# Performance work log

Hardware: AMD Instinct MI355X
Metric: run time of the kernel (lower is better)

The kernel has to match this reference:

```python
import jax, jax.numpy as jnp
import numpy as np

B, M, HS, K = 2, 2048, 1024, 16
D = HS // K


def setup_inputs() -> dict:
    key = jax.random.key(0)
    k1, k2, k3, k4 = jax.random.split(key, 4)
    s = 1.0 / np.sqrt(HS)
    return {
        "h": jax.random.normal(k1, (B, M, HS), jnp.float32),
        "W_span": jax.random.normal(k2, (2 * K, HS), jnp.float32) * s,
        "W_val": jax.random.normal(k3, (HS, HS), jnp.float32) * s,
        "W_out": jax.random.normal(k4, (HS, HS), jnp.float32) * s,
    }


def _head_reshape(x, d):
    # (B, M, K*d) -> (B*K, M, d), matching torch view/transpose in head_reshape
    b, m, _ = x.shape
    return x.reshape(b, m, K, d).transpose(0, 2, 1, 3).reshape(b * K, m, d)


def reference(h, W_span, W_val, W_out):
    b, m, hs = h.shape
    span = _head_reshape(h @ W_span.T, 2)        # (B*K, M, 2)
    value = _head_reshape(h @ W_val.T, D)        # (B*K, M, D)
    # AutoSelectAttention: learned per-position Gaussian span over absolute positions
    pos = jnp.arange(m, dtype=h.dtype)           # (M,)
    mean = jax.nn.sigmoid(span[..., 0]) * m      # (B*K, M) span center in [0, M]
    soft = jax.nn.softplus(span[..., 1])         # (B*K, M) sharpness >= 0
    diff = pos[None, None, :] - mean[..., None]  # (B*K, M, M)
    scores = -soft[..., None] * (diff * diff)
    attn = jax.nn.softmax(scores, axis=-1)       # (B*K, M, M)
    out = jnp.matmul(attn, value)                # (B*K, M, D)
    out = out.reshape(b, K, m, D).transpose(0, 2, 1, 3).reshape(b, m, hs)
    return out @ W_out.T
```

## Files before the change

### kernel.cpp

```cpp
#include <hip/hip_runtime.h>
#include <hip/hip_bf16.h>

#define MM   2048
#define HSZ  1024
#define KH   16
#define DH   64

typedef __attribute__((ext_vector_type(8))) short bf16x8;
typedef __attribute__((ext_vector_type(4))) float f32x4;
typedef __attribute__((ext_vector_type(8))) unsigned short u16x8;

#define GLOAD_LDS16(gp, lp) \
    __builtin_amdgcn_global_load_lds( \
        (const __attribute__((address_space(1))) unsigned int*)(gp), \
        (__attribute__((address_space(3))) unsigned int*)(lp), 16, 0, 0)

__device__ __forceinline__ unsigned short f2bf(float x) {
    union { float f; unsigned u; } v; v.f = x;
    unsigned r = v.u + 0x7FFFu + ((v.u >> 16) & 1u);
    return (unsigned short)(r >> 16);
}

__global__ __launch_bounds__(256) void span_cvt(
    const float* __restrict__ h, const float* __restrict__ Wspan,
    const float* __restrict__ Wval, const float* __restrict__ Wout,
    float* __restrict__ mean_, float* __restrict__ soft_,
    unsigned short* __restrict__ h_bf,
    unsigned short* __restrict__ Wval_bf, unsigned short* __restrict__ Wout_bf)
{
    __shared__ float hrow[4][HSZ];
    int t = threadIdx.x;

    if (blockIdx.x >= 1024) {
        int bid = blockIdx.x - 1024;
        const float* in = (bid < 1024) ? Wval : Wout;
        unsigned short* out = (bid < 1024) ? Wval_bf : Wout_bf;
        int i = ((bid & 1023) * 256 + t) * 4;
        float4 v = *(const float4*)(in + i);
        ushort4 o;
        o.x = f2bf(v.x); o.y = f2bf(v.y); o.z = f2bf(v.z); o.w = f2bf(v.w);
        *(ushort4*)(out + i) = o;
        return;
    }

    int row0 = blockIdx.x * 4;
    #pragma unroll
    for (int i = 0; i < 4; ++i) {
        int li = t + 256 * i;
        int r = li >> 8, c4 = (li & 255) * 4;
        float4 hv = *(const float4*)&h[(long)(row0 + r) * HSZ + c4];
        *(float4*)&hrow[r][c4] = hv;
        ushort4 hb;
        hb.x = f2bf(hv.x); hb.y = f2bf(hv.y); hb.z = f2bf(hv.z); hb.w = f2bf(hv.w);
        *(ushort4*)&h_bf[(long)(row0 + r) * HSZ + c4] = hb;
    }
    __syncthreads();
    int o = t >> 3, part = t & 7;
    const float* w = Wspan + o * HSZ;
    float4 acc[4] = {};
    #pragma unroll 4
    for (int i = 0; i < 32; ++i) {
        int c = part * 4 + i * 32;
        float4 wv = *(const float4*)&w[c];
        #pragma unroll
        for (int r = 0; r < 4; ++r) {
            float4 a = *(const float4*)&hrow[r][c];
            acc[r].x += a.x * wv.x; acc[r].y += a.y * wv.y;
            acc[r].z += a.z * wv.z; acc[r].w += a.w * wv.w;
        }
    }
    #pragma unroll
    for (int r = 0; r < 4; ++r) {
        float s = acc[r].x + acc[r].y + acc[r].z + acc[r].w;
        s += __shfl_xor(s, 1, 64);
        s += __shfl_xor(s, 2, 64);
        s += __shfl_xor(s, 4, 64);
        if (part == 0) {
            int m = row0 + r;
            int b = m >> 11, mm = m & 2047;
            int bk = b * KH + (o >> 1);
            if ((o & 1) == 0) {
                mean_[bk * MM + mm] = (1.f / (1.f + __expf(-s))) * (float)MM;
            } else {
                float sp = (s > 15.f) ? s : log1pf(__expf(s));
                soft_[bk * MM + mm] = sp;
            }
        }
    }
}

#define SROW(li) ((li) >> 3)
#define SCOL(li) ((((li) & 7) ^ (SROW(li) & 7)) * 8)

template<int STORE_BF16>
__device__ __forceinline__ void gemm_core64(
    unsigned short* __restrict__ AsB, unsigned short* __restrict__ BsB,
    const unsigned short* __restrict__ A, const unsigned short* __restrict__ Bm,
    void* __restrict__ Cv, int N, int Kd,
    int bx, int by, int bz, long aZ, long bZ, long cZ)
{
    const unsigned short* Ab = A  + bz * aZ;
    const unsigned short* Bb = Bm + bz * bZ;
    long czoff = bz * cZ;
    int row0 = by * 64;
    int col0 = bx * 64;
    int t = threadIdx.x;
    int wid = t >> 6, l = t & 63;
    int wr = wid >> 1, wc = wid & 1;
    int lr = l & 15, lhi = l >> 4;

    #define STAGE64(buf, k0s) do { \
        unsigned short* As_ = AsB + (buf) * 4096; \
        unsigned short* Bs_ = BsB + (buf) * 4096; \
        int a0 = t, a1 = t + 256; \
        GLOAD_LDS16(Ab + (long)(row0 + SROW(a0)) * Kd + (k0s) + SCOL(a0), As_ + a0 * 8); \
        GLOAD_LDS16(Ab + (long)(row0 + SROW(a1)) * Kd + (k0s) + SCOL(a1), As_ + a1 * 8); \
        GLOAD_LDS16(Bb + (long)(col0 + SROW(a0)) * Kd + (k0s) + SCOL(a0), Bs_ + a0 * 8); \
        GLOAD_LDS16(Bb + (long)(col0 + SROW(a1)) * Kd + (k0s) + SCOL(a1), Bs_ + a1 * 8); \
    } while (0)

    f32x4 acc[2][2] = {};
    int nk = Kd >> 6;

    STAGE64(0, 0);

    for (int ks = 0; ks < nk; ++ks) {
        int cur = ks & 1;
        if (ks + 1 < nk) {
            STAGE64(cur ^ 1, (ks + 1) << 6);
            asm volatile("s_waitcnt vmcnt(4)" ::: "memory");
        } else {
            asm volatile("s_waitcnt vmcnt(0)" ::: "memory");
        }
        __builtin_amdgcn_s_barrier();

        bf16x8 af[2][2], bfr[2][2];
        #pragma unroll
        for (int kk = 0; kk < 2; ++kk) {
            int slotx = ((kk * 4 + lhi) ^ (lr & 7)) << 3;
            #pragma unroll
            for (int i = 0; i < 2; ++i)
                af[kk][i] = *(const bf16x8*)(AsB + cur * 4096 + (wr * 32 + i * 16 + lr) * 64 + slotx);
            #pragma unroll
            for (int j = 0; j < 2; ++j)
                bfr[kk][j] = *(const bf16x8*)(BsB + cur * 4096 + (wc * 32 + j * 16 + lr) * 64 + slotx);
        }
        asm volatile("s_waitcnt lgkmcnt(0)" ::: "memory");
        __builtin_amdgcn_sched_barrier(0);
        __builtin_amdgcn_s_barrier();

        #pragma unroll
        for (int kk = 0; kk < 2; ++kk)
            #pragma unroll
            for (int i = 0; i < 2; ++i)
                #pragma unroll
                for (int j = 0; j < 2; ++j)
                    acc[i][j] = __builtin_amdgcn_mfma_f32_16x16x32_bf16(af[kk][i], bfr[kk][j], acc[i][j], 0, 0, 0);
    }
    #undef STAGE64

    #pragma unroll
    for (int i = 0; i < 2; ++i) {
        int rbase = row0 + wr * 32 + i * 16 + lhi * 4;
        #pragma unroll
        for (int j = 0; j < 2; ++j) {
            int cidx = col0 + wc * 32 + j * 16 + lr;
            #pragma unroll
            for (int r_ = 0; r_ < 4; ++r_) {
                long idx = czoff + (long)(rbase + r_) * N + cidx;
                if (STORE_BF16) ((unsigned short*)Cv)[idx] = f2bf(acc[i][j][r_]);
                else            ((float*)Cv)[idx] = acc[i][j][r_];
            }
        }
    }
}

__device__ void sort_core(char* smem, const float* __restrict__ mean_,
                          int* __restrict__ perm, int bk)
{
    unsigned short (*hist)[257] = (unsigned short(*)[257])smem;
    int* binTot = (int*)(smem + 16448);
    int* binStart = binTot + 32;
    int t = threadIdx.x;
    int bins[8];
    #pragma unroll
    for (int i = 0; i < 8; ++i) {
        float mq = mean_[bk * MM + t * 8 + i];
        int b = (int)(mq * (1.f / 64.f));
        bins[i] = min(31, max(0, b));
    }
    for (int b = 0; b < 32; ++b) hist[b][t] = 0;
    __syncthreads();
    #pragma unroll
    for (int i = 0; i < 8; ++i) hist[bins[i]][t]++;
    __syncthreads();
    int w = t >> 6, l = t & 63;
    for (int b = w * 8; b < w * 8 + 8; ++b) {
        int carry = 0;
        for (int g = 0; g < 4; ++g) {
            int v = (int)hist[b][g * 64 + l];
            int x = v;
            #pragma unroll
            for (int off = 1; off < 64; off <<= 1) {
                int y = __shfl_up(x, off, 64);
                if (l >= off) x += y;
            }
            hist[b][g * 64 + l] = (unsigned short)(x - v + carry);
            carry += __shfl(x, 63, 64);
        }
        if (l == 0) binTot[b] = carry;
    }
    __syncthreads();
    if (t == 0) {
        int s = 0;
        for (int b = 0; b < 32; ++b) { binStart[b] = s; s += binTot[b]; }
    }
    __syncthreads();
    #pragma unroll
    for (int i = 0; i < 8; ++i) {
        int b = bins[i];
        int prior = 0;
        #pragma unroll
        for (int j = 0; j < 8; ++j) if (j < i && bins[j] == b) prior++;
        int pos = binStart[b] + (int)hist[b][t] + prior;
        perm[bk * MM + pos] = t * 8 + i;
    }
}

__global__ __launch_bounds__(256) void vgemm_sort(
    const unsigned short* __restrict__ Wval_bf, const unsigned short* __restrict__ h_bf,
    unsigned short* __restrict__ hvT,
    const float* __restrict__ mean_, int* __restrict__ perm)
{
    __shared__ __align__(16) char smem[32768];
    int f = blockIdx.x;
    if (f < 1024) {
        int swz = (f & 7) * 128 + (f >> 3);
        int by = swz & 15, r = swz >> 4;
        int bx = r & 31, bz = r >> 5;
        gemm_core64<1>((unsigned short*)smem, (unsigned short*)(smem + 16384),
                       Wval_bf, h_bf, hvT, MM, HSZ, bx, by, bz,
                       0L, (long)MM * HSZ, (long)HSZ * MM);
    } else {
        sort_core(smem, mean_, perm, f - 1024);
    }
}

__global__ __launch_bounds__(256) void ogemm(
    const unsigned short* __restrict__ att, const unsigned short* __restrict__ Wout_bf,
    float* __restrict__ out)
{
    __shared__ __align__(16) unsigned short As[2][4096];
    __shared__ __align__(16) unsigned short Bs[2][4096];
    int f = blockIdx.x;
    int swz = (f & 7) * 128 + (f >> 3);
    int bx = swz & 15, by = (swz >> 4) & 63;
    gemm_core64<0>(&As[0][0], &Bs[0][0], att, Wout_bf, out, HSZ, HSZ,
                   bx, by, 0, 0L, 0L, 0L);
}

__global__ __launch_bounds__(512) void attn_gauss(
    const float* __restrict__ mean_, const float* __restrict__ soft_,
    const int* __restrict__ perm,
    const unsigned short* __restrict__ hvT, unsigned short* __restrict__ att)
{
    __shared__ __align__(16) unsigned short Vs[2][64 * 64];
    __shared__ float red[2][8];
    int flat = blockIdx.x;
    int swz = (flat & 7) * 64 + (flat >> 3);
    int bk = swz >> 4;
    int qb = swz & 15;
    int t = threadIdx.x, wid = t >> 6, l = t & 63;
    int b = bk >> 4, head = bk & 15;
    int lr = l & 15, lhi = l >> 4;
    int slot = qb * 128 + wid * 16 + lr;
    int q = perm[bk * MM + slot];
    float mq  = mean_[bk * MM + q];
    float sq  = soft_[bk * MM + q];
    const unsigned short* Vbase = hvT + (long)bk * DH * MM;

    float w = __fsqrt_rn(50.f / sq);
    float lo = mq - w, hi = mq + w;
    #pragma unroll
    for (int off = 1; off < 64; off <<= 1) {
        lo = fminf(lo, __shfl_xor(lo, off, 64));
        hi = fmaxf(hi, __shfl_xor(hi, off, 64));
    }
    if (l == 0) { red[0][wid] = lo; red[1][wid] = hi; }
    __syncthreads();
    float blo = red[0][0], bhi = red[1][0];
    #pragma unroll
    for (int i = 1; i < 8; ++i) {
        blo = fminf(blo, red[0][i]);
        bhi = fmaxf(bhi, red[1][i]);
    }
    blo = fmaxf(blo, 0.f);
    bhi = fmaxf(fminf(bhi, 2047.f), 0.f);
    int kt0 = ((int)blo) >> 6;
    int kt1 = ((int)bhi) >> 6;
    if (kt1 < kt0) kt1 = kt0;

    int sr = t >> 3;
    int sc = (((t & 7) ^ (sr & 7)) * 8);

    f32x4 acc[4] = {};
    float lsum = 0.f;
    int jlane0 = lhi * 8;

    GLOAD_LDS16(Vbase + (long)sr * MM + (kt0 << 6) + sc, &Vs[0][t * 8]);
    __syncthreads();

    for (int kt = kt0; kt <= kt1; ++kt) {
        int cur = (kt - kt0) & 1;
        int k0 = kt << 6;
        if (kt < kt1)
            GLOAD_LDS16(Vbase + (long)sr * MM + (k0 + 64) + sc, &Vs[cur ^ 1][t * 8]);

        float dmin = fmaxf(fmaxf((float)k0 - mq, mq - (float)(k0 + 63)), 0.f);
        bool active = (sq * dmin * dmin) < 50.f;
        if (__ballot(active)) {
            #pragma unroll
            for (int kk = 0; kk < 64; kk += 32) {
                bf16x8 pfrag;
                float dbase = (float)(k0 + kk + jlane0) - mq;
                #pragma unroll
                for (int jj = 0; jj < 8; ++jj) {
                    float d_ = dbase + (float)jj;
                    float p = __expf(-sq * d_ * d_);
                    lsum += p;
                    pfrag[jj] = (short)f2bf(p);
                }
                int slotx = (((kk >> 3) + lhi) ^ (lr & 7)) << 3;
                #pragma unroll
                for (int df = 0; df < 4; ++df) {
                    bf16x8 vf = *(const bf16x8*)&Vs[cur][(df * 16 + lr) * 64 + slotx];
                    acc[df] = __builtin_amdgcn_mfma_f32_16x16x32_bf16(pfrag, vf, acc[df], 0, 0, 0);
                }
            }
        }
        __syncthreads();
    }

    lsum += __shfl_xor(lsum, 16, 64);
    lsum += __shfl_xor(lsum, 32, 64);

    int slot_base = qb * 128 + wid * 16;
    #pragma unroll
    for (int r_ = 0; r_ < 4; ++r_) {
        int qr = lhi * 4 + r_;
        float inv = 1.f / __shfl(lsum, qr, 64);
        int qo = perm[bk * MM + slot_base + qr];
        long orow = ((long)b * MM + qo) * HSZ + head * DH;
        #pragma unroll
        for (int df = 0; df < 4; ++df)
            att[orow + df * 16 + lr] = f2bf(acc[df][r_] * inv);
    }
}

extern "C" void kernel_launch(void* const* d_in, const int* in_sizes, int n_in,
                              void* d_out, int out_size, void* d_ws, size_t ws_size,
                              hipStream_t stream) {
    (void)in_sizes; (void)n_in; (void)out_size; (void)ws_size;
    const float* h     = (const float*)d_in[0];
    const float* Wspan = (const float*)d_in[1];
    const float* Wval  = (const float*)d_in[2];
    const float* Wout  = (const float*)d_in[3];
    float* out = (float*)d_out;

    char* ws = (char*)d_ws;
    unsigned short* h_bf    = (unsigned short*)(ws);
    unsigned short* Wval_bf = (unsigned short*)(ws +  8388608);
    unsigned short* Wout_bf = (unsigned short*)(ws + 10485760);
    unsigned short* hvT     = (unsigned short*)(ws + 12582912);
    unsigned short* att     = (unsigned short*)(ws + 20971520);
    float*          mean_   = (float*)(ws + 29360128);
    float*          soft_   = (float*)(ws + 29622272);
    int*            perm    = (int*)(ws + 29884416);

    span_cvt<<<3072, 256, 0, stream>>>(h, Wspan, Wval, Wout,
                                       mean_, soft_, h_bf, Wval_bf, Wout_bf);

    vgemm_sort<<<1056, 256, 0, stream>>>(Wval_bf, h_bf, hvT, mean_, perm);

    attn_gauss<<<512, 512, 0, stream>>>(mean_, soft_, perm, hvT, att);

    ogemm<<<1024, 256, 0, stream>>>(att, Wout_bf, out);
}
```

Baseline: 66.39 us.

## Compute span projection with split-bf16 MFMA and shrink conversion grid

Replaces the scalar FP32 dot-product span projection with MFMA 16x16x32 bf16 instructions. It keeps near-FP32 accuracy by splitting h and W_span into hi and lo bf16 parts and issuing three MFMAs per step, with W_span staged in swizzled LDS. The launch drops from 3072 to 256 blocks: 128 blocks handle 32 rows each, and 128 blocks convert the weights with a 16-iteration loop. This cuts instruction count and launch overhead, at the cost of 128 KB of LDS per block, which limits occupancy.

Result: slower. 68.96 us (+3.9%).

```diff
diff --git a/kernel.cpp b/kernel.cpp
--- a/kernel.cpp
+++ b/kernel.cpp
@@ -28,63 +28,108 @@
     unsigned short* __restrict__ h_bf,
     unsigned short* __restrict__ Wval_bf, unsigned short* __restrict__ Wout_bf)
 {
-    __shared__ float hrow[4][HSZ];
+    __shared__ __align__(16) unsigned short Whi[32768];
+    __shared__ __align__(16) unsigned short Wlo[32768];
     int t = threadIdx.x;
 
-    if (blockIdx.x >= 1024) {
-        int bid = blockIdx.x - 1024;
-        const float* in = (bid < 1024) ? Wval : Wout;
-        unsigned short* out = (bid < 1024) ? Wval_bf : Wout_bf;
-        int i = ((bid & 1023) * 256 + t) * 4;
-        float4 v = *(const float4*)(in + i);
-        ushort4 o;
-        o.x = f2bf(v.x); o.y = f2bf(v.y); o.z = f2bf(v.z); o.w = f2bf(v.w);
-        *(ushort4*)(out + i) = o;
+    if (blockIdx.x >= 128) {
+        int bid = blockIdx.x - 128;
+        #pragma unroll 4
+        for (int it = 0; it < 16; ++it) {
+            int fi = bid * 256 + t + it * 32768;
+            const float* in; unsigned short* out; int off;
+            if (fi < 262144) { in = Wval; out = Wval_bf; off = fi; }
+            else             { in = Wout; out = Wout_bf; off = fi - 262144; }
+            float4 v = *(const float4*)(in + (long)off * 4);
+            ushort4 o4;
+            o4.x = f2bf(v.x); o4.y = f2bf(v.y); o4.z = f2bf(v.z); o4.w = f2bf(v.w);
+            *(ushort4*)(out + (long)off * 4) = o4;
+        }
         return;
     }
 
-    int row0 = blockIdx.x * 4;
-    #pragma unroll
-    for (int i = 0; i < 4; ++i) {
-        int li = t + 256 * i;
-        int r = li >> 8, c4 = (li & 255) * 4;
-        float4 hv = *(const float4*)&h[(long)(row0 + r) * HSZ + c4];
-        *(float4*)&hrow[r][c4] = hv;
-        ushort4 hb;
-        hb.x = f2bf(hv.x); hb.y = f2bf(hv.y); hb.z = f2bf(hv.z); hb.w = f2bf(hv.w);
-        *(ushort4*)&h_bf[(long)(row0 + r) * HSZ + c4] = hb;
-    }
-    __syncthreads();
-    int o = t >> 3, part = t & 7;
-    const float* w = Wspan + o * HSZ;
-    float4 acc[4] = {};
-    #pragma unroll 4
-    for (int i = 0; i < 32; ++i) {
-        int c = part * 4 + i * 32;
-        float4 wv = *(const float4*)&w[c];
-        #pragma unroll
-        for (int r = 0; r < 4; ++r) {
-            float4 a = *(const float4*)&hrow[r][c];
-            acc[r].x += a.x * wv.x; acc[r].y += a.y * wv.y;
-            acc[r].z += a.z * wv.z; acc[r].w += a.w * wv.w;
-        }
-    }
-    #pragma unroll
-    for (int r = 0; r < 4; ++r) {
-        float s = acc[r].x + acc[r].y + acc[r].z + acc[r].w;
-        s += __shfl_xor(s, 1, 64);
-        s += __shfl_xor(s, 2, 64);
-        s += __shfl_xor(s, 4, 64);
-        if (part == 0) {
-            int m = row0 + r;
-            int b = m >> 11, mm = m & 2047;
-            int bk = b * KH + (o >> 1);
-            if ((o & 1) == 0) {
-                mean_[bk * MM + mm] = (1.f / (1.f + __expf(-s))) * (float)MM;
-            } else {
-                float sp = (s > 15.f) ? s : log1pf(__expf(s));
-                soft_[bk * MM + mm] = sp;
-            }
+    #pragma unroll
+    for (int g = 0; g < 16; ++g) {
+        int idx = t + 256 * g;
+        int o = idx >> 7, kc = idx & 127;
+        const float* wp = Wspan + o * 1024 + kc * 8;
+        float4 w0 = *(const float4*)wp;
+        float4 w1 = *(const float4*)(wp + 4);
+        float wf[8] = {w0.x, w0.y, w0.z, w0.w, w1.x, w1.y, w1.z, w1.w};
+        u16x8 hv_, lv_;
+        #pragma unroll
+        for (int jj = 0; jj < 8; ++jj) {
+            unsigned short hu = f2bf(wf[jj]);
+            union { unsigned u; float f; } c; c.u = (unsigned)hu << 16;
+            hv_[jj] = hu;
+            lv_[jj] = f2bf(wf[jj] - c.f);
+        }
+        int slot = (o * 128 + (kc ^ (o & 7))) * 8;
+        *(u16x8*)&Whi[slot] = hv_;
+        *(u16x8*)&Wlo[slot] = lv_;
+    }
+    __syncthreads();
+
+    int wid = t >> 6, l = t & 63;
+    int lr = l & 15, lhi = l >> 4;
+    int rgrp = wid >> 1, jt = wid & 1;
+    int arow = blockIdx.x * 32 + rgrp * 16 + lr;
+    const float* hp = h + (long)arow * HSZ;
+    unsigned short* hbp = h_bf + (long)arow * HSZ;
+    int o = jt * 16 + lr;
+    int wbase = o * 128, osw = o & 7;
+
+    f32x4 acc = {};
+
+    #define PROC(a, b, ks_) do { \
+        float af_[8] = {(a).x, (a).y, (a).z, (a).w, (b).x, (b).y, (b).z, (b).w}; \
+        bf16x8 hh_, hl_; \
+        _Pragma("unroll") \
+        for (int jj = 0; jj < 8; ++jj) { \
+            unsigned short hu_ = f2bf(af_[jj]); \
+            union { unsigned u; float f; } c_; c_.u = (unsigned)hu_ << 16; \
+            hh_[jj] = (short)hu_; \
+            hl_[jj] = (short)f2bf(af_[jj] - c_.f); \
+        } \
+        if (jt == 0) *(bf16x8*)(hbp + (ks_) * 32 + lhi * 8) = hh_; \
+        int kc_ = (ks_) * 4 + lhi; \
+        int slot_ = (wbase + (kc_ ^ osw)) * 8; \
+        bf16x8 whi_ = *(const bf16x8*)&Whi[slot_]; \
+        bf16x8 wlo_ = *(const bf16x8*)&Wlo[slot_]; \
+        acc = __builtin_amdgcn_mfma_f32_16x16x32_bf16(hh_, whi_, acc, 0, 0, 0); \
+        acc = __builtin_amdgcn_mfma_f32_16x16x32_bf16(hh_, wlo_, acc, 0, 0, 0); \
+        acc = __builtin_amdgcn_mfma_f32_16x16x32_bf16(hl_, whi_, acc, 0, 0, 0); \
+    } while (0)
+
+    float4 A0a = *(const float4*)(hp + lhi * 8);
+    float4 A0b = *(const float4*)(hp + lhi * 8 + 4);
+    float4 A1a = *(const float4*)(hp + 32 + lhi * 8);
+    float4 A1b = *(const float4*)(hp + 32 + lhi * 8 + 4);
+    for (int ks = 0; ks < 32; ks += 2) {
+        float4 N0a, N0b, N1a, N1b;
+        if (ks + 2 < 32) {
+            const float* p0 = hp + (ks + 2) * 32 + lhi * 8;
+            const float* p1 = hp + (ks + 3) * 32 + lhi * 8;
+            N0a = *(const float4*)p0; N0b = *(const float4*)(p0 + 4);
+            N1a = *(const float4*)p1; N1b = *(const float4*)(p1 + 4);
+        }
+        PROC(A0a, A0b, ks);
+        PROC(A1a, A1b, ks + 1);
+        A0a = N0a; A0b = N0b; A1a = N1a; A1b = N1b;
+    }
+    #undef PROC
+
+    #pragma unroll
+    for (int r_ = 0; r_ < 4; ++r_) {
+        int m = blockIdx.x * 32 + rgrp * 16 + lhi * 4 + r_;
+        int b = m >> 11, mm = m & 2047;
+        int bk = b * KH + (o >> 1);
+        float s = acc[r_];
+        if (!(o & 1)) {
+            mean_[bk * MM + mm] = (1.f / (1.f + __expf(-s))) * (float)MM;
+        } else {
+            float sp = (s > 15.f) ? s : log1pf(__expf(s));
+            soft_[bk * MM + mm] = sp;
         }
     }
 }
@@ -377,8 +422,8 @@
     float*          soft_   = (float*)(ws + 29622272);
     int*            perm    = (int*)(ws + 29884416);
 
-    span_cvt<<<3072, 256, 0, stream>>>(h, Wspan, Wval, Wout,
-                                       mean_, soft_, h_bf, Wval_bf, Wout_bf);
+    span_cvt<<<256, 256, 0, stream>>>(h, Wspan, Wval, Wout,
+                                      mean_, soft_, h_bf, Wval_bf, Wout_bf);
 
     vgemm_sort<<<1056, 256, 0, stream>>>(Wval_bf, h_bf, hvT, mean_, perm);
 
```

## Fuse bf16 conversion into value GEMM and move span sort into attention

Applied to the files above, without the earlier changes.

The value GEMM now loads fp32 h and W_val directly, converts them to bf16 in registers and writes them into swizzled LDS. This removes the separate h_bf/Wval_bf conversion pass and its global round trip, and the span projection runs in the same launch interleaved with the GEMM blocks. The per-head sort of span centers moves into the attention kernel, which keeps the permutation in LDS and drops one kernel launch and the perm buffer. The cost is that each of the 512 attention blocks redoes its own sort, and the GEMM loses async global-to-LDS loads in favour of register staging with full vmcnt waits. The conversion also switches to a cheaper round-half-up instead of round-to-nearest-even.

Result: slower. 100.2 us (+50.9%).

```diff
diff --git a/kernel.cpp b/kernel.cpp
--- a/kernel.cpp
+++ b/kernel.cpp
@@ -20,71 +20,167 @@
     unsigned r = v.u + 0x7FFFu + ((v.u >> 16) & 1u);
     return (unsigned short)(r >> 16);
 }
-
-__global__ __launch_bounds__(256) void span_cvt(
+__device__ __forceinline__ unsigned short f2bfu(float x) {
+    union { float f; unsigned u; } v; v.f = x;
+    return (unsigned short)((v.u + 0x8000u) >> 16);
+}
+__device__ __forceinline__ u16x8 pack8(float4 a, float4 b) {
+    u16x8 o;
+    o[0] = f2bfu(a.x); o[1] = f2bfu(a.y); o[2] = f2bfu(a.z); o[3] = f2bfu(a.w);
+    o[4] = f2bfu(b.x); o[5] = f2bfu(b.y); o[6] = f2bfu(b.z); o[7] = f2bfu(b.w);
+    return o;
+}
+
+__global__ __launch_bounds__(256) void fused1(
     const float* __restrict__ h, const float* __restrict__ Wspan,
     const float* __restrict__ Wval, const float* __restrict__ Wout,
     float* __restrict__ mean_, float* __restrict__ soft_,
-    unsigned short* __restrict__ h_bf,
-    unsigned short* __restrict__ Wval_bf, unsigned short* __restrict__ Wout_bf)
+    unsigned short* __restrict__ hvT, unsigned short* __restrict__ Wout_bf)
 {
-    __shared__ float hrow[4][HSZ];
+    __shared__ __align__(16) char smem[32768];
+    int f = blockIdx.x;
     int t = threadIdx.x;
 
-    if (blockIdx.x >= 1024) {
-        int bid = blockIdx.x - 1024;
-        const float* in = (bid < 1024) ? Wval : Wout;
-        unsigned short* out = (bid < 1024) ? Wval_bf : Wout_bf;
-        int i = ((bid & 1023) * 256 + t) * 4;
-        float4 v = *(const float4*)(in + i);
-        ushort4 o;
-        o.x = f2bf(v.x); o.y = f2bf(v.y); o.z = f2bf(v.z); o.w = f2bf(v.w);
-        *(ushort4*)(out + i) = o;
+    if (f >= 2048) {
+        int bid = f - 2048;
+        #pragma unroll
+        for (int it = 0; it < 8; ++it) {
+            int fi = bid * 2048 + t + it * 256;
+            float4 v = *(const float4*)(Wout + (long)fi * 4);
+            ushort4 o4;
+            o4.x = f2bf(v.x); o4.y = f2bf(v.y); o4.z = f2bf(v.z); o4.w = f2bf(v.w);
+            *(ushort4*)(Wout_bf + (long)fi * 4) = o4;
+        }
         return;
     }
 
-    int row0 = blockIdx.x * 4;
+    if (f & 1) {
+        float (*hrow)[HSZ] = (float(*)[HSZ])smem;
+        int row0 = (f >> 1) * 4;
+        #pragma unroll
+        for (int i = 0; i < 4; ++i) {
+            int li = t + 256 * i;
+            int r = li >> 8, c4 = (li & 255) * 4;
+            *(float4*)&hrow[r][c4] = *(const float4*)&h[(long)(row0 + r) * HSZ + c4];
+        }
+        __syncthreads();
+        int o = t >> 3, part = t & 7;
+        const float* w = Wspan + o * HSZ;
+        float4 acc[4] = {};
+        #pragma unroll 4
+        for (int i = 0; i < 32; ++i) {
+            int c = part * 4 + i * 32;
+            float4 wv = *(const float4*)&w[c];
+            #pragma unroll
+            for (int r = 0; r < 4; ++r) {
+                float4 a = *(const float4*)&hrow[r][c];
+                acc[r].x += a.x * wv.x; acc[r].y += a.y * wv.y;
+                acc[r].z += a.z * wv.z; acc[r].w += a.w * wv.w;
+            }
+        }
+        #pragma unroll
+        for (int r = 0; r < 4; ++r) {
+            float s = acc[r].x + acc[r].y + acc[r].z + acc[r].w;
+            s += __shfl_xor(s, 1, 64);
+            s += __shfl_xor(s, 2, 64);
+            s += __shfl_xor(s, 4, 64);
+            if (part == 0) {
+                int m = row0 + r;
+                int b = m >> 11, mm = m & 2047;
+                int bk = b * KH + (o >> 1);
+                if ((o & 1) == 0) {
+                    mean_[bk * MM + mm] = (1.f / (1.f + __expf(-s))) * (float)MM;
+                } else {
+                    float sp = (s > 15.f) ? s : log1pf(__expf(s));
+                    soft_[bk * MM + mm] = sp;
+                }
+            }
+        }
+        return;
+    }
+
+    unsigned short* As = (unsigned short*)smem;
+    unsigned short* Bs = (unsigned short*)(smem + 16384);
+    int g = f >> 1;
+    int swz = (g & 7) * 128 + (g >> 3);
+    int by = swz & 15; int r_ = swz >> 4;
+    int bx = r_ & 31, bz = r_ >> 5;
+    int wid = t >> 6, l = t & 63;
+    int wr = wid >> 1, wc = wid & 1;
+    int lr = l & 15, lhi = l >> 4;
+
+    int srow = t >> 2, sk = (t & 3) * 16;
+    const float* Ap = Wval + (long)(by * 64 + srow) * HSZ + sk;
+    const float* Bp = h + (long)bz * MM * HSZ + (long)(bx * 64 + srow) * HSZ + sk;
+    int c0 = (t & 3) * 2;
+    int p0 = ((c0 ^ (srow & 7)) * 8), p1 = (((c0 + 1) ^ (srow & 7)) * 8);
+    int wbase = srow * 64;
+
+    #define LOADG(RA, RB, kt) do { \
+        _Pragma("unroll") for (int j_ = 0; j_ < 4; ++j_) { \
+            RA[j_] = *(const float4*)(Ap + (kt) * 64 + j_ * 4); \
+            RB[j_] = *(const float4*)(Bp + (kt) * 64 + j_ * 4); } } while (0)
+    #define CVTW(RA, RB, buf) do { \
+        *(u16x8*)&As[(buf) * 4096 + wbase + p0] = pack8(RA[0], RA[1]); \
+        *(u16x8*)&As[(buf) * 4096 + wbase + p1] = pack8(RA[2], RA[3]); \
+        *(u16x8*)&Bs[(buf) * 4096 + wbase + p0] = pack8(RB[0], RB[1]); \
+        *(u16x8*)&Bs[(buf) * 4096 + wbase + p1] = pack8(RB[2], RB[3]); } while (0)
+
+    f32x4 acc[2][2] = {};
+    #define STEP(buf) do { \
+        bf16x8 af[2][2], bfr[2][2]; \
+        _Pragma("unroll") for (int kk = 0; kk < 2; ++kk) { \
+            int slotx = ((kk * 4 + lhi) ^ (lr & 7)) << 3; \
+            _Pragma("unroll") for (int i_ = 0; i_ < 2; ++i_) \
+                af[kk][i_] = *(const bf16x8*)&As[(buf) * 4096 + (wr * 32 + i_ * 16 + lr) * 64 + slotx]; \
+            _Pragma("unroll") for (int j_ = 0; j_ < 2; ++j_) \
+                bfr[kk][j_] = *(const bf16x8*)&Bs[(buf) * 4096 + (wc * 32 + j_ * 16 + lr) * 64 + slotx]; } \
+        asm volatile("s_waitcnt lgkmcnt(0)" ::: "memory"); \
+        __builtin_amdgcn_sched_barrier(0); \
+        _Pragma("unroll") for (int kk = 0; kk < 2; ++kk) \
+            _Pragma("unroll") for (int i_ = 0; i_ < 2; ++i_) \
+                _Pragma("unroll") for (int j_ = 0; j_ < 2; ++j_) \
+                    acc[i_][j_] = __builtin_amdgcn_mfma_f32_16x16x32_bf16(af[kk][i_], bfr[kk][j_], acc[i_][j_], 0, 0, 0); \
+    } while (0)
+
+    float4 A0[4], B0[4], A1[4], B1[4];
+    LOADG(A0, B0, 0);
+    asm volatile("s_waitcnt vmcnt(0)" ::: "memory");
+    CVTW(A0, B0, 0);
+    LOADG(A1, B1, 1);
+    __syncthreads();
+
+    for (int ks = 0; ks < 16; ks += 2) {
+        if (ks + 1 < 16) {
+            asm volatile("s_waitcnt vmcnt(0)" ::: "memory");
+            CVTW(A1, B1, 1);
+            if (ks + 2 < 16) LOADG(A0, B0, ks + 2);
+        }
+        STEP(0);
+        __syncthreads();
+        if (ks + 2 < 16) {
+            asm volatile("s_waitcnt vmcnt(0)" ::: "memory");
+            CVTW(A0, B0, 0);
+            if (ks + 3 < 16) LOADG(A1, B1, ks + 3);
+        }
+        STEP(1);
+        __syncthreads();
+    }
+    #undef LOADG
+    #undef CVTW
+    #undef STEP
+
+    long czoff = (long)bz * HSZ * MM;
+    int row0 = by * 64, col0 = bx * 64;
     #pragma unroll
-    for (int i = 0; i < 4; ++i) {
-        int li = t + 256 * i;
-        int r = li >> 8, c4 = (li & 255) * 4;
-        float4 hv = *(const float4*)&h[(long)(row0 + r) * HSZ + c4];
-        *(float4*)&hrow[r][c4] = hv;
-        ushort4 hb;
-        hb.x = f2bf(hv.x); hb.y = f2bf(hv.y); hb.z = f2bf(hv.z); hb.w = f2bf(hv.w);
-        *(ushort4*)&h_bf[(long)(row0 + r) * HSZ + c4] = hb;
-    }
-    __syncthreads();
-    int o = t >> 3, part = t & 7;
-    const float* w = Wspan + o * HSZ;
-    float4 acc[4] = {};
-    #pragma unroll 4
-    for (int i = 0; i < 32; ++i) {
-        int c = part * 4 + i * 32;
-        float4 wv = *(const float4*)&w[c];
-        #pragma unroll
-        for (int r = 0; r < 4; ++r) {
-            float4 a = *(const float4*)&hrow[r][c];
-            acc[r].x += a.x * wv.x; acc[r].y += a.y * wv.y;
-            acc[r].z += a.z * wv.z; acc[r].w += a.w * wv.w;
-        }
-    }
-    #pragma unroll
-    for (int r = 0; r < 4; ++r) {
-        float s = acc[r].x + acc[r].y + acc[r].z + acc[r].w;
-        s += __shfl_xor(s, 1, 64);
-        s += __shfl_xor(s, 2, 64);
-        s += __shfl_xor(s, 4, 64);
-        if (part == 0) {
-            int m = row0 + r;
-            int b = m >> 11, mm = m & 2047;
-            int bk = b * KH + (o >> 1);
-            if ((o & 1) == 0) {
-                mean_[bk * MM + mm] = (1.f / (1.f + __expf(-s))) * (float)MM;
-            } else {
-                float sp = (s > 15.f) ? s : log1pf(__expf(s));
-                soft_[bk * MM + mm] = sp;
-            }
+    for (int i = 0; i < 2; ++i) {
+        int rbase = row0 + wr * 32 + i * 16 + lhi * 4;
+        #pragma unroll
+        for (int j = 0; j < 2; ++j) {
+            int cidx = col0 + wc * 32 + j * 16 + lr;
+            #pragma unroll
+            for (int rr = 0; rr < 4; ++rr)
+                hvT[czoff + (long)(rbase + rr) * MM + cidx] = f2bf(acc[i][j][rr]);
         }
     }
 }
@@ -92,16 +188,11 @@
 #define SROW(li) ((li) >> 3)
 #define SCOL(li) ((((li) & 7) ^ (SROW(li) & 7)) * 8)
 
-template<int STORE_BF16>
-__device__ __forceinline__ void gemm_core64(
+__device__ __forceinline__ void gemm_core64_f32out(
     unsigned short* __restrict__ AsB, unsigned short* __restrict__ BsB,
     const unsigned short* __restrict__ A, const unsigned short* __restrict__ Bm,
-    void* __restrict__ Cv, int N, int Kd,
-    int bx, int by, int bz, long aZ, long bZ, long cZ)
+    float* __restrict__ Cv, int N, int Kd, int bx, int by)
 {
-    const unsigned short* Ab = A  + bz * aZ;
-    const unsigned short* Bb = Bm + bz * bZ;
-    long czoff = bz * cZ;
     int row0 = by * 64;
     int col0 = bx * 64;
     int t = threadIdx.x;
@@ -113,17 +204,15 @@
         unsigned short* As_ = AsB + (buf) * 4096; \
         unsigned short* Bs_ = BsB + (buf) * 4096; \
         int a0 = t, a1 = t + 256; \
-        GLOAD_LDS16(Ab + (long)(row0 + SROW(a0)) * Kd + (k0s) + SCOL(a0), As_ + a0 * 8); \
-        GLOAD_LDS16(Ab + (long)(row0 + SROW(a1)) * Kd + (k0s) + SCOL(a1), As_ + a1 * 8); \
-        GLOAD_LDS16(Bb + (long)(col0 + SROW(a0)) * Kd + (k0s) + SCOL(a0), Bs_ + a0 * 8); \
-        GLOAD_LDS16(Bb + (long)(col0 + SROW(a1)) * Kd + (k0s) + SCOL(a1), Bs_ + a1 * 8); \
+        GLOAD_LDS16(A + (long)(row0 + SROW(a0)) * Kd + (k0s) + SCOL(a0), As_ + a0 * 8); \
+        GLOAD_LDS16(A + (long)(row0 + SROW(a1)) * Kd + (k0s) + SCOL(a1), As_ + a1 * 8); \
+        GLOAD_LDS16(Bm + (long)(col0 + SROW(a0)) * Kd + (k0s) + SCOL(a0), Bs_ + a0 * 8); \
+        GLOAD_LDS16(Bm + (long)(col0 + SROW(a1)) * Kd + (k0s) + SCOL(a1), Bs_ + a1 * 8); \
     } while (0)
 
     f32x4 acc[2][2] = {};
     int nk = Kd >> 6;
-
     STAGE64(0, 0);
-
     for (int ks = 0; ks < nk; ++ks) {
         int cur = ks & 1;
         if (ks + 1 < nk) {
@@ -166,83 +255,9 @@
         for (int j = 0; j < 2; ++j) {
             int cidx = col0 + wc * 32 + j * 16 + lr;
             #pragma unroll
-            for (int r_ = 0; r_ < 4; ++r_) {
-                long idx = czoff + (long)(rbase + r_) * N + cidx;
-                if (STORE_BF16) ((unsigned short*)Cv)[idx] = f2bf(acc[i][j][r_]);
-                else            ((float*)Cv)[idx] = acc[i][j][r_];
-            }
-        }
-    }
-}
-
-__device__ void sort_core(char* smem, const float* __restrict__ mean_,
-                          int* __restrict__ perm, int bk)
-{
-    unsigned short (*hist)[257] = (unsigned short(*)[257])smem;
-    int* binTot = (int*)(smem + 16448);
-    int* binStart = binTot + 32;
-    int t = threadIdx.x;
-    int bins[8];
-    #pragma unroll
-    for (int i = 0; i < 8; ++i) {
-        float mq = mean_[bk * MM + t * 8 + i];
-        int b = (int)(mq * (1.f / 64.f));
-        bins[i] = min(31, max(0, b));
-    }
-    for (int b = 0; b < 32; ++b) hist[b][t] = 0;
-    __syncthreads();
-    #pragma unroll
-    for (int i = 0; i < 8; ++i) hist[bins[i]][t]++;
-    __syncthreads();
-    int w = t >> 6, l = t & 63;
-    for (int b = w * 8; b < w * 8 + 8; ++b) {
-        int carry = 0;
-        for (int g = 0; g < 4; ++g) {
-            int v = (int)hist[b][g * 64 + l];
-            int x = v;
-            #pragma unroll
-            for (int off = 1; off < 64; off <<= 1) {
-                int y = __shfl_up(x, off, 64);
-                if (l >= off) x += y;
-            }
-            hist[b][g * 64 + l] = (unsigned short)(x - v + carry);
-            carry += __shfl(x, 63, 64);
-        }
-        if (l == 0) binTot[b] = carry;
-    }
-    __syncthreads();
-    if (t == 0) {
-        int s = 0;
-        for (int b = 0; b < 32; ++b) { binStart[b] = s; s += binTot[b]; }
-    }
-    __syncthreads();
-    #pragma unroll
-    for (int i = 0; i < 8; ++i) {
-        int b = bins[i];
-        int prior = 0;
-        #pragma unroll
-        for (int j = 0; j < 8; ++j) if (j < i && bins[j] == b) prior++;
-        int pos = binStart[b] + (int)hist[b][t] + prior;
-        perm[bk * MM + pos] = t * 8 + i;
-    }
-}
-
-__global__ __launch_bounds__(256) void vgemm_sort(
-    const unsigned short* __restrict__ Wval_bf, const unsigned short* __restrict__ h_bf,
-    unsigned short* __restrict__ hvT,
-    const float* __restrict__ mean_, int* __restrict__ perm)
-{
-    __shared__ __align__(16) char smem[32768];
-    int f = blockIdx.x;
-    if (f < 1024) {
-        int swz = (f & 7) * 128 + (f >> 3);
-        int by = swz & 15, r = swz >> 4;
-        int bx = r & 31, bz = r >> 5;
-        gemm_core64<1>((unsigned short*)smem, (unsigned short*)(smem + 16384),
-                       Wval_bf, h_bf, hvT, MM, HSZ, bx, by, bz,
-                       0L, (long)MM * HSZ, (long)HSZ * MM);
-    } else {
-        sort_core(smem, mean_, perm, f - 1024);
+            for (int rr = 0; rr < 4; ++rr)
+                Cv[(long)(rbase + rr) * N + cidx] = acc[i][j][rr];
+        }
     }
 }
 
@@ -255,16 +270,15 @@
     int f = blockIdx.x;
     int swz = (f & 7) * 128 + (f >> 3);
     int bx = swz & 15, by = (swz >> 4) & 63;
-    gemm_core64<0>(&As[0][0], &Bs[0][0], att, Wout_bf, out, HSZ, HSZ,
-                   bx, by, 0, 0L, 0L, 0L);
+    gemm_core64_f32out(&As[0][0], &Bs[0][0], att, Wout_bf, out, HSZ, HSZ, bx, by);
 }
 
 __global__ __launch_bounds__(512) void attn_gauss(
     const float* __restrict__ mean_, const float* __restrict__ soft_,
-    const int* __restrict__ perm,
     const unsigned short* __restrict__ hvT, unsigned short* __restrict__ att)
 {
-    __shared__ __align__(16) unsigned short Vs[2][64 * 64];
+    __shared__ __align__(16) char usm[16704];
+    __shared__ int permL[2048];
     __shared__ float red[2][8];
     int flat = blockIdx.x;
     int swz = (flat & 7) * 64 + (flat >> 3);
@@ -273,10 +287,68 @@
     int t = threadIdx.x, wid = t >> 6, l = t & 63;
     int b = bk >> 4, head = bk & 15;
     int lr = l & 15, lhi = l >> 4;
+
+    {
+        unsigned short (*hist)[257] = (unsigned short(*)[257])usm;
+        int* binTot = (int*)(usm + 16448);
+        int* binStart = binTot + 32;
+        int bins[8];
+        if (t < 256) {
+            #pragma unroll
+            for (int i = 0; i < 8; ++i) {
+                float mq_ = mean_[bk * MM + t * 8 + i];
+                int bb = (int)(mq_ * (1.f / 64.f));
+                bins[i] = min(31, max(0, bb));
+            }
+            for (int bb = 0; bb < 32; ++bb) hist[bb][t] = 0;
+        }
+        __syncthreads();
+        if (t < 256) {
+            #pragma unroll
+            for (int i = 0; i < 8; ++i) hist[bins[i]][t]++;
+        }
+        __syncthreads();
+        if (wid < 4) {
+            for (int bb = wid * 8; bb < wid * 8 + 8; ++bb) {
+                int carry = 0;
+                for (int g = 0; g < 4; ++g) {
+                    int v = (int)hist[bb][g * 64 + l];
+                    int x = v;
+                    #pragma unroll
+                    for (int off = 1; off < 64; off <<= 1) {
+                        int y = __shfl_up(x, off, 64);
+                        if (l >= off) x += y;
+                    }
+                    hist[bb][g * 64 + l] = (unsigned short)(x - v + carry);
+                    carry += __shfl(x, 63, 64);
+                }
+                if (l == 0) binTot[bb] = carry;
+            }
+        }
+        __syncthreads();
+        if (t == 0) {
+            int s = 0;
+            for (int bb = 0; bb < 32; ++bb) { binStart[bb] = s; s += binTot[bb]; }
+        }
+        __syncthreads();
+        if (t < 256) {
+            #pragma unroll
+            for (int i = 0; i < 8; ++i) {
+                int bb = bins[i];
+                int prior = 0;
+                #pragma unroll
+                for (int j = 0; j < 8; ++j) if (j < i && bins[j] == bb) prior++;
+                permL[binStart[bb] + (int)hist[bb][t] + prior] = t * 8 + i;
+            }
+        }
+        __syncthreads();
+    }
+
+    unsigned short (*Vs)[4096] = (unsigned short(*)[4096])usm;
     int slot = qb * 128 + wid * 16 + lr;
-    int q = perm[bk * MM + slot];
-    float mq  = mean_[bk * MM + q];
-    float sq  = soft_[bk * MM + q];
+    int q = permL[slot];
+    float mq = mean_[bk * MM + q];
+    float sq = soft_[bk * MM + q];
     const unsigned short* Vbase = hvT + (long)bk * DH * MM;
 
     float w = __fsqrt_rn(50.f / sq);
@@ -349,7 +421,7 @@
     for (int r_ = 0; r_ < 4; ++r_) {
         int qr = lhi * 4 + r_;
         float inv = 1.f / __shfl(lsum, qr, 64);
-        int qo = perm[bk * MM + slot_base + qr];
+        int qo = permL[slot_base + qr];
         long orow = ((long)b * MM + qo) * HSZ + head * DH;
         #pragma unroll
         for (int df = 0; df < 4; ++df)
@@ -368,21 +440,16 @@
     float* out = (float*)d_out;
 
     char* ws = (char*)d_ws;
-    unsigned short* h_bf    = (unsigned short*)(ws);
-    unsigned short* Wval_bf = (unsigned short*)(ws +  8388608);
-    unsigned short* Wout_bf = (unsigned short*)(ws + 10485760);
-    unsigned short* hvT     = (unsigned short*)(ws + 12582912);
-    unsigned short* att     = (unsigned short*)(ws + 20971520);
-    float*          mean_   = (float*)(ws + 29360128);
-    float*          soft_   = (float*)(ws + 29622272);
-    int*            perm    = (int*)(ws + 29884416);
-
-    span_cvt<<<3072, 256, 0, stream>>>(h, Wspan, Wval, Wout,
-                                       mean_, soft_, h_bf, Wval_bf, Wout_bf);
-
-    vgemm_sort<<<1056, 256, 0, stream>>>(Wval_bf, h_bf, hvT, mean_, perm);
-
-    attn_gauss<<<512, 512, 0, stream>>>(mean_, soft_, perm, hvT, att);
+    unsigned short* hvT     = (unsigned short*)(ws);
+    unsigned short* att     = (unsigned short*)(ws +  8388608);
+    unsigned short* Wout_bf = (unsigned short*)(ws + 16777216);
+    float*          mean_   = (float*)(ws + 18874368);
+    float*          soft_   = (float*)(ws + 19136512);
+
+    fused1<<<2176, 256, 0, stream>>>(h, Wspan, Wval, Wout,
+                                     mean_, soft_, hvT, Wout_bf);
+
+    attn_gauss<<<512, 512, 0, stream>>>(mean_, soft_, hvT, att);
 
     ogemm<<<1024, 256, 0, stream>>>(att, Wout_bf, out);
 }
```

## Compute span projection with split-bf16 MFMA and separate conversion blocks

Applied to the files above, without the earlier changes.

The first kernel's span projection (h @ W_span^T) is rewritten. Previously scalar FP32 dot products ran over 4 rows per block. Now 64 blocks each handle 64 rows using bf16 MFMA with hi/lo splitting to keep near-fp32 accuracy, and a triple-buffered global-to-LDS pipeline feeds them. The h, Wval and Wout bf16 conversion moves to 1536 separate blocks that process 4 float4s per thread. This cuts the block count and replaces slow FP32 ALU work with matrix cores, but only 64 blocks carry the 16-step serial projection loop and may become the tail.

Result: slower. 69.70 us (+5.0%).

```diff
diff --git a/kernel.cpp b/kernel.cpp
--- a/kernel.cpp
+++ b/kernel.cpp
@@ -21,70 +21,124 @@
     return (unsigned short)(r >> 16);
 }
 
-__global__ __launch_bounds__(256) void span_cvt(
+__global__ __launch_bounds__(256) void pre_fused(
     const float* __restrict__ h, const float* __restrict__ Wspan,
     const float* __restrict__ Wval, const float* __restrict__ Wout,
     float* __restrict__ mean_, float* __restrict__ soft_,
     unsigned short* __restrict__ h_bf,
     unsigned short* __restrict__ Wval_bf, unsigned short* __restrict__ Wout_bf)
 {
-    __shared__ float hrow[4][HSZ];
+    __shared__ __align__(16) float As[3][64 * 64];
+    __shared__ __align__(16) unsigned short Whi[2][32 * 64];
+    __shared__ __align__(16) unsigned short Wlo[2][32 * 64];
     int t = threadIdx.x;
 
-    if (blockIdx.x >= 1024) {
-        int bid = blockIdx.x - 1024;
-        const float* in = (bid < 1024) ? Wval : Wout;
-        unsigned short* out = (bid < 1024) ? Wval_bf : Wout_bf;
-        int i = ((bid & 1023) * 256 + t) * 4;
-        float4 v = *(const float4*)(in + i);
-        ushort4 o;
-        o.x = f2bf(v.x); o.y = f2bf(v.y); o.z = f2bf(v.z); o.w = f2bf(v.w);
-        *(ushort4*)(out + i) = o;
+    if (blockIdx.x >= 64) {
+        int bid = blockIdx.x - 64;
+        #pragma unroll
+        for (int i = 0; i < 4; ++i) {
+            int fi = bid * 1024 + i * 256 + t;
+            const float* in; unsigned short* out; int off;
+            if (fi < 1048576)      { in = h;    out = h_bf;    off = fi; }
+            else if (fi < 1310720) { in = Wval; out = Wval_bf; off = fi - 1048576; }
+            else                   { in = Wout; out = Wout_bf; off = fi - 1310720; }
+            float4 v = *(const float4*)(in + (long)off * 4);
+            ushort4 o4;
+            o4.x = f2bf(v.x); o4.y = f2bf(v.y); o4.z = f2bf(v.z); o4.w = f2bf(v.w);
+            *(ushort4*)(out + (long)off * 4) = o4;
+        }
         return;
     }
 
-    int row0 = blockIdx.x * 4;
-    #pragma unroll
-    for (int i = 0; i < 4; ++i) {
-        int li = t + 256 * i;
-        int r = li >> 8, c4 = (li & 255) * 4;
-        float4 hv = *(const float4*)&h[(long)(row0 + r) * HSZ + c4];
-        *(float4*)&hrow[r][c4] = hv;
-        ushort4 hb;
-        hb.x = f2bf(hv.x); hb.y = f2bf(hv.y); hb.z = f2bf(hv.z); hb.w = f2bf(hv.w);
-        *(ushort4*)&h_bf[(long)(row0 + r) * HSZ + c4] = hb;
-    }
-    __syncthreads();
-    int o = t >> 3, part = t & 7;
-    const float* w = Wspan + o * HSZ;
-    float4 acc[4] = {};
-    #pragma unroll 4
-    for (int i = 0; i < 32; ++i) {
-        int c = part * 4 + i * 32;
-        float4 wv = *(const float4*)&w[c];
-        #pragma unroll
-        for (int r = 0; r < 4; ++r) {
-            float4 a = *(const float4*)&hrow[r][c];
-            acc[r].x += a.x * wv.x; acc[r].y += a.y * wv.y;
-            acc[r].z += a.z * wv.z; acc[r].w += a.w * wv.w;
-        }
-    }
-    #pragma unroll
-    for (int r = 0; r < 4; ++r) {
-        float s = acc[r].x + acc[r].y + acc[r].z + acc[r].w;
-        s += __shfl_xor(s, 1, 64);
-        s += __shfl_xor(s, 2, 64);
-        s += __shfl_xor(s, 4, 64);
-        if (part == 0) {
-            int m = row0 + r;
+    int row0 = blockIdx.x * 64;
+    int wid = t >> 6, l = t & 63;
+    int lr = l & 15, lhi = l >> 4;
+    int arow = wid * 16 + lr;
+    int wo = t >> 3, wc8 = t & 7;
+    const float* wsrc = Wspan + wo * 1024 + wc8 * 8;
+    int wdst = wo * 64 + ((wc8 ^ (wo & 7)) * 8);
+
+    f32x4 acc[2] = {};
+    float4 WA0, WA1, WB0, WB1;
+
+    #define WLOAD(R0, R1, k0) { R0 = *(const float4*)(wsrc + (k0)); \
+                                R1 = *(const float4*)(wsrc + (k0) + 4); }
+    #define STAGEA(buf, k0) { \
+        _Pragma("unroll") for (int i_ = 0; i_ < 4; ++i_) { \
+            int li = t + 256 * i_; int rw = li >> 4; int cs = li & 15; \
+            GLOAD_LDS16(h + (long)(row0 + rw) * HSZ + (k0) + ((cs ^ (rw & 15)) * 4), \
+                        &As[buf][li * 4]); } }
+    #define WWRITE(buf, R0, R1) { \
+        float wf_[8] = {R0.x,R0.y,R0.z,R0.w,R1.x,R1.y,R1.z,R1.w}; \
+        u16x8 hi8, lo8; \
+        _Pragma("unroll") for (int j_ = 0; j_ < 8; ++j_) { \
+            unsigned short hu_ = f2bf(wf_[j_]); \
+            union { unsigned u; float f; } cv_; cv_.u = (unsigned)hu_ << 16; \
+            hi8[j_] = hu_; lo8[j_] = f2bf(wf_[j_] - cv_.f); } \
+        *(u16x8*)&Whi[buf][wdst] = hi8; *(u16x8*)&Wlo[buf][wdst] = lo8; }
+    #define COMPUTE(abuf, wbuf) { \
+        _Pragma("unroll") for (int ksub = 0; ksub < 2; ++ksub) { \
+            int c_ = ksub * 8 + lhi * 2; \
+            int s0_ = c_ ^ (arow & 15), s1_ = (c_ + 1) ^ (arow & 15); \
+            float4 fa_ = *(const float4*)&As[abuf][arow * 64 + s0_ * 4]; \
+            float4 fb_ = *(const float4*)&As[abuf][arow * 64 + s1_ * 4]; \
+            float af_[8] = {fa_.x,fa_.y,fa_.z,fa_.w,fb_.x,fb_.y,fb_.z,fb_.w}; \
+            bf16x8 hh_, hl_; \
+            _Pragma("unroll") for (int j_ = 0; j_ < 8; ++j_) { \
+                unsigned short hu_ = f2bf(af_[j_]); \
+                union { unsigned u; float f; } cv_; cv_.u = (unsigned)hu_ << 16; \
+                hh_[j_] = (short)hu_; hl_[j_] = (short)f2bf(af_[j_] - cv_.f); } \
+            _Pragma("unroll") for (int ct_ = 0; ct_ < 2; ++ct_) { \
+                int orow_ = ct_ * 16 + lr; \
+                int ws_ = ((ksub * 4 + lhi) ^ (orow_ & 7)) * 8; \
+                bf16x8 wh_ = *(const bf16x8*)&Whi[wbuf][orow_ * 64 + ws_]; \
+                bf16x8 wl_ = *(const bf16x8*)&Wlo[wbuf][orow_ * 64 + ws_]; \
+                acc[ct_] = __builtin_amdgcn_mfma_f32_16x16x32_bf16(hh_, wh_, acc[ct_], 0, 0, 0); \
+                acc[ct_] = __builtin_amdgcn_mfma_f32_16x16x32_bf16(hh_, wl_, acc[ct_], 0, 0, 0); \
+                acc[ct_] = __builtin_amdgcn_mfma_f32_16x16x32_bf16(hl_, wh_, acc[ct_], 0, 0, 0); } } }
+
+    WLOAD(WA0, WA1, 0);
+    STAGEA(0, 0);
+    WLOAD(WB0, WB1, 64);
+    STAGEA(1, 64);
+    asm volatile("s_waitcnt vmcnt(6)" ::: "memory");
+    WWRITE(0, WA0, WA1);
+    asm volatile("s_waitcnt lgkmcnt(0)" ::: "memory");
+    __builtin_amdgcn_s_barrier();
+
+    #pragma unroll
+    for (int ks = 0; ks < 16; ++ks) {
+        if (ks + 2 < 16) {
+            if ((ks & 1) == 0) { WLOAD(WA0, WA1, (ks + 2) * 64); }
+            else               { WLOAD(WB0, WB1, (ks + 2) * 64); }
+            STAGEA((ks + 2) % 3, (ks + 2) * 64);
+        }
+        if (ks + 2 < 16) asm volatile("s_waitcnt vmcnt(4)" ::: "memory");
+        else             asm volatile("s_waitcnt vmcnt(0)" ::: "memory");
+        if (ks + 1 < 16) {
+            if (ks & 1) WWRITE((ks + 1) & 1, WA0, WA1)
+            else        WWRITE((ks + 1) & 1, WB0, WB1)
+        }
+        COMPUTE(ks % 3, ks & 1);
+        asm volatile("s_waitcnt lgkmcnt(0)" ::: "memory");
+        __builtin_amdgcn_s_barrier();
+    }
+    #undef WLOAD
+    #undef STAGEA
+    #undef WWRITE
+    #undef COMPUTE
+
+    #pragma unroll
+    for (int ct = 0; ct < 2; ++ct) {
+        int o = ct * 16 + lr;
+        #pragma unroll
+        for (int r_ = 0; r_ < 4; ++r_) {
+            int m = row0 + wid * 16 + lhi * 4 + r_;
             int b = m >> 11, mm = m & 2047;
             int bk = b * KH + (o >> 1);
-            if ((o & 1) == 0) {
-                mean_[bk * MM + mm] = (1.f / (1.f + __expf(-s))) * (float)MM;
-            } else {
-                float sp = (s > 15.f) ? s : log1pf(__expf(s));
-                soft_[bk * MM + mm] = sp;
-            }
+            float s = acc[ct][r_];
+            if (!(o & 1)) mean_[bk * MM + mm] = (1.f / (1.f + __expf(-s))) * (float)MM;
+            else          soft_[bk * MM + mm] = (s > 15.f) ? s : log1pf(__expf(s));
         }
     }
 }
@@ -377,8 +431,8 @@
     float*          soft_   = (float*)(ws + 29622272);
     int*            perm    = (int*)(ws + 29884416);
 
-    span_cvt<<<3072, 256, 0, stream>>>(h, Wspan, Wval, Wout,
-                                       mean_, soft_, h_bf, Wval_bf, Wout_bf);
+    pre_fused<<<1600, 256, 0, stream>>>(h, Wspan, Wval, Wout,
+                                        mean_, soft_, h_bf, Wval_bf, Wout_bf);
 
     vgemm_sort<<<1056, 256, 0, stream>>>(Wval_bf, h_bf, hvT, mean_, perm);
 
```
